# Optimization experiments

Hardware: AMD Instinct MI355X
Metric: run time of the kernel (lower is better)

The kernel has to match this reference:

```python
import jax, jax.numpy as jnp
import numpy as np

IN_CH = 128
OUT_CH = 256
KSIZE = 3
DOWN = 2
WSCALE_GAIN = 1.0
LR_MUL = 1.0
ACT_GAIN = float(np.sqrt(2.0))  # lrelu def_gain
CONV_CLAMP = 256.0
LRELU_SLOPE = 0.2


def _setup_filter():
    # upfirdn2d.setup_filter([1,3,3,1]): normalize 1D then outer product -> 2D
    f1 = jnp.asarray([1.0, 3.0, 3.0, 1.0], dtype=jnp.float32)
    f1 = f1 / jnp.sum(f1)
    f2 = jnp.outer(f1, f1)  # [4,4]
    return f2


def setup_inputs() -> dict:
    key = jax.random.key(0)
    k1, k2 = jax.random.split(key)
    x = jax.random.normal(k1, (16, IN_CH, 256, 256), dtype=jnp.float32)
    weight = jax.random.normal(k2, (OUT_CH, IN_CH, KSIZE, KSIZE), dtype=jnp.float32)
    bias = jnp.zeros((OUT_CH,), dtype=jnp.float32)
    return {"x": x, "weight": weight, "bias": bias}


def reference(x, weight, bias):
    # runtime_gain = 1.0
    fan_in = KSIZE * KSIZE * IN_CH
    wscale = WSCALE_GAIN / np.sqrt(fan_in) * LR_MUL  # use_wscale=True
    w = weight * jnp.float32(wscale)
    b = bias * jnp.float32(LR_MUL)

    # filter_padding for k=3, fh=fw=4, down=2 -> (2,2,2,2) as (left,right,top,bottom)
    pad = (KSIZE // 2 + (4 - DOWN + 1) // 2, KSIZE // 2 + (4 - DOWN) // 2)
    # upfirdn2d(x, f, down=1, padding): pad then correlate with flipped filter
    f2 = _setup_filter()
    f2 = f2[::-1, ::-1]  # flip (symmetric here, kept for faithfulness)
    C = x.shape[1]
    fk = jnp.broadcast_to(f2[None, None], (C, 1, 4, 4))  # depthwise kernel
    x = lax.pad_fn(x, pad) if False else jnp.pad(x, ((0, 0), (0, 0), (pad[1], pad[0]) if False else (pad[0], pad[1]), (pad[0], pad[1])))
    x = jax.lax.conv_general_dilated(
        x, fk, window_strides=(1, 1), padding='VALID',
        dimension_numbers=('NCHW', 'OIHW', 'NCHW'),
        feature_group_count=C)

    # strided conv2d, padding=0, stride=down
    x = jax.lax.conv_general_dilated(
        x, w, window_strides=(DOWN, DOWN), padding='VALID',
        dimension_numbers=('NCHW', 'OIHW', 'NCHW'))

    # fused bias + lrelu + gain + clamp
    x = x + b[None, :, None, None]
    x = jnp.where(x >= 0, x, x * jnp.float32(LRELU_SLOPE)) * jnp.float32(ACT_GAIN)
    x = jnp.clip(x, -jnp.float32(CONV_CLAMP), jnp.float32(CONV_CLAMP))
    return x
```

## Files before the change

### kernel.cpp

```cpp
#include <hip/hip_runtime.h>

typedef __attribute__((ext_vector_type(8))) short bf16x8;
typedef __attribute__((ext_vector_type(4))) float f32x4;
typedef __attribute__((ext_vector_type(2))) float f32x2;
typedef __attribute__((ext_vector_type(4))) unsigned int u32x4;

static __device__ __forceinline__ unsigned short f2bf(float f) {
    union { float f; unsigned u; } v; v.f = f;
    return (unsigned short)((v.u + 0x7FFFu + ((v.u >> 16) & 1u)) >> 16);
}

static __device__ __forceinline__ void g2l16(const void* g, void* l) {
    __builtin_amdgcn_global_load_lds(
        (const __attribute__((address_space(1))) unsigned int*)g,
        (__attribute__((address_space(3))) unsigned int*)l, 16, 0, 0);
}

__global__ void prep_weights(const float* __restrict__ w, unsigned short* __restrict__ wp) {
    int t = blockIdx.x * 256 + threadIdx.x;
    const float wscale = 0.02946278254943948f;
    int cw = t & 31;
    int oc = (t >> 5) & 255;
    int cr = t >> 13;
    int ch = cr / 9;
    int rs = cr - ch * 9;
    int r  = rs / 3;
    int s  = rs - r * 3;
    int c  = ch * 32 + cw;
    wp[t] = f2bf(w[((oc * 128 + c) * 3 + r) * 3 + s] * wscale);
}

#define BRW(ROW) {                                                             \
    int _xr = xr0 + (ROW);                                                     \
    int _xc = _xr < 0 ? 0 : (_xr > 255 ? 255 : _xr);                           \
    float _rm = (_xr == _xc) ? 0.125f : 0.0f;                                  \
    const float* _q0 = p0lo + (_xc << 8);                                      \
    const float* _h0p = p0hi + (_xc << 8);                                     \
    const float* _q1 = p1lo + (_xc << 8);                                      \
    const float* _h1p = p1hi + (_xc << 8);                                     \
    f32x4 _l0, _l1; f32x2 _h0, _h1;                                            \
    __builtin_memcpy(&_l0, _q0, 16); __builtin_memcpy(&_h0, _h0p, 8);          \
    __builtin_memcpy(&_l1, _q1, 16); __builtin_memcpy(&_h1, _h1p, 8);          \
    float w00 = eL ? 0.f : _l0.x,  w01 = eL ? 0.f : _l0.y;                     \
    float w02 = eL ? _l0.x : _l0.z, w03 = eL ? _l0.y : _l0.w;                  \
    float w04 = eR ? 0.f : (eL ? _l0.z : _h0.x);                               \
    float w05 = eR ? 0.f : (eL ? _l0.w : _h0.y);                               \
    float w10 = eL ? 0.f : _l1.x,  w11 = eL ? 0.f : _l1.y;                     \
    float w12 = eL ? _l1.x : _l1.z, w13 = eL ? _l1.y : _l1.w;                  \
    float w14 = eR ? 0.f : (eL ? _l1.z : _h1.x);                               \
    float w15 = eR ? 0.f : (eL ? _l1.w : _h1.y);                               \
    hA0[(ROW) & 3] = (w00 + 3.f * (w01 + w02) + w03) * _rm;                    \
    hB0[(ROW) & 3] = (w01 + 3.f * (w02 + w03) + w04) * _rm;                    \
    hC0[(ROW) & 3] = (w02 + 3.f * (w03 + w04) + w05) * _rm;                    \
    hA1[(ROW) & 3] = (w10 + 3.f * (w11 + w12) + w13) * _rm;                    \
    hB1[(ROW) & 3] = (w11 + 3.f * (w12 + w13) + w14) * _rm;                    \
    hC1[(ROW) & 3] = (w12 + 3.f * (w13 + w14) + w15) * _rm;                    \
}
#define BWV(ROW) {                                                             \
    float vA0 = (hA0[(ROW-3)&3] + 3.f*(hA0[(ROW-2)&3]+hA0[(ROW-1)&3]) + hA0[(ROW)&3]) * 0.125f; \
    float vA1 = (hA1[(ROW-3)&3] + 3.f*(hA1[(ROW-2)&3]+hA1[(ROW-1)&3]) + hA1[(ROW)&3]) * 0.125f; \
    float vB0 = (hB0[(ROW-3)&3] + 3.f*(hB0[(ROW-2)&3]+hB0[(ROW-1)&3]) + hB0[(ROW)&3]) * 0.125f; \
    float vB1 = (hB1[(ROW-3)&3] + 3.f*(hB1[(ROW-2)&3]+hB1[(ROW-1)&3]) + hB1[(ROW)&3]) * 0.125f; \
    unsigned _rb = (unsigned)(ROW - 3) * 2112u;                                \
    *(unsigned*)(blds + _rb + o0) = (unsigned)f2bf(vA0) | ((unsigned)f2bf(vA1) << 16); \
    *(unsigned*)(blds + _rb + o1) = (unsigned)f2bf(vB0) | ((unsigned)f2bf(vB1) << 16); \
    if (a15) {                                                                 \
        float vC0 = (hC0[(ROW-3)&3] + 3.f*(hC0[(ROW-2)&3]+hC0[(ROW-1)&3]) + hC0[(ROW)&3]) * 0.125f; \
        float vC1 = (hC1[(ROW-3)&3] + 3.f*(hC1[(ROW-2)&3]+hC1[(ROW-1)&3]) + hC1[(ROW)&3]) * 0.125f; \
        *(unsigned*)(blds + _rb + o2) = (unsigned)f2bf(vC0) | ((unsigned)f2bf(vC1) << 16); \
    }                                                                          \
}

__global__ __launch_bounds__(512, 4)
void blur_rec(const float* __restrict__ x, unsigned char* __restrict__ bm) {
    __shared__ __align__(16) unsigned char blds[17 * 2112];

    const int braw = blockIdx.x;
    const int bx   = ((braw & 7) << 10) | (braw >> 3);
    const int cg   = bx & 3;
    const int tile = (bx >> 2) & 127;
    const int n    = bx >> 9;
    const int u0   = (tile >> 3) * 8;
    const int v0   = (tile & 7) * 16;
    const int tid  = threadIdx.x;
    const int a    = tid & 15;
    const int chp  = (tid >> 4) & 15;
    const int h    = tid >> 8;
    const bool a15 = (a == 15);
    const int wc   = 2 * v0 - 2 + 2 * a;
    const bool eL  = (v0 == 0 && a == 0);
    const bool eR  = (v0 == 112 && a15);
    const int colLo = eL ? 0 : wc;
    const int colHi = eR ? 248 : (wc + 4);
    const float* plane0 = x + (size_t)(n * 128 + cg * 32 + 2 * chp) * 65536;
    const float* p0lo = plane0 + colLo;
    const float* p0hi = plane0 + colHi;
    const float* p1lo = p0lo + 65536;
    const float* p1hi = p0hi + 65536;
    const int xr0 = 2 * u0 - 2;

    const int J0 = 2 * a, J1 = 2 * a + 1;
    const unsigned cb2 = (unsigned)(chp & 3) * 4u;
    const unsigned o0 = (unsigned)((J0 ^ ((J0 >> 1) & 1)) * 64)
                      + ((((unsigned)chp >> 2) ^ (((unsigned)J0 >> 2) & 3u)) << 4) + cb2;
    const unsigned o1 = (unsigned)((J1 ^ ((J1 >> 1) & 1)) * 64)
                      + ((((unsigned)chp >> 2) ^ (((unsigned)J1 >> 2) & 3u)) << 4) + cb2;
    const unsigned o2 = 2048u + (((unsigned)chp >> 2) << 4) + cb2;

    {
        float hA0[4], hB0[4], hC0[4], hA1[4], hB1[4], hC1[4];
        if (h == 0) {
            BRW(0) BRW(1) BRW(2)
            BRW(3)  BWV(3)   BRW(4)  BWV(4)   BRW(5)  BWV(5)
            BRW(6)  BWV(6)   BRW(7)  BWV(7)   BRW(8)  BWV(8)
            BRW(9)  BWV(9)   BRW(10) BWV(10)  BRW(11) BWV(11)
        } else {
            BRW(9) BRW(10) BRW(11)
            BRW(12) BWV(12)  BRW(13) BWV(13)  BRW(14) BWV(14)
            BRW(15) BWV(15)  BRW(16) BWV(16)  BRW(17) BWV(17)
            BRW(18) BWV(18)  BRW(19) BWV(19)
        }
    }
    __syncthreads();
    unsigned char* dst = bm + (size_t)bx * 35904u;
    #pragma unroll
    for (int k = 0; k < 5; ++k) {
        int sl = tid + 512 * k;
        if (sl < 2244)
            *(u32x4*)(dst + (unsigned)sl * 16u) = *(const u32x4*)(blds + (unsigned)sl * 16u);
    }
}

#define MF __builtin_amdgcn_mfma_f32_16x16x32_bf16
#define WLOAD2(S0, S1, KOFF) {                                                 \
    const unsigned short* _wn = wbase + (size_t)(KOFF) * 8192;                 \
    S0 = *(const bf16x8*)(_wn); S1 = *(const bf16x8*)(_wn + 512);              \
}
#define CSTEP8(BUF, ADRS, R, S0, S1) {                                         \
    const unsigned char* _ab = lds + (BUF) + (ADRS) + (R) * 2112;              \
    bf16x8 a0 = *(const bf16x8*)(_ab);                                         \
    bf16x8 a1 = *(const bf16x8*)(_ab +  4224);                                 \
    bf16x8 a2 = *(const bf16x8*)(_ab +  8448);                                 \
    bf16x8 a3 = *(const bf16x8*)(_ab + 12672);                                 \
    bf16x8 a4 = *(const bf16x8*)(_ab + 16896);                                 \
    bf16x8 a5 = *(const bf16x8*)(_ab + 21120);                                 \
    bf16x8 a6 = *(const bf16x8*)(_ab + 25344);                                 \
    bf16x8 a7 = *(const bf16x8*)(_ab + 29568);                                 \
    __builtin_amdgcn_s_setprio(1);                                             \
    acc[0][0]=MF(a0,S0,acc[0][0],0,0,0); acc[0][1]=MF(a0,S1,acc[0][1],0,0,0);  \
    acc[1][0]=MF(a1,S0,acc[1][0],0,0,0); acc[1][1]=MF(a1,S1,acc[1][1],0,0,0);  \
    acc[2][0]=MF(a2,S0,acc[2][0],0,0,0); acc[2][1]=MF(a2,S1,acc[2][1],0,0,0);  \
    acc[3][0]=MF(a3,S0,acc[3][0],0,0,0); acc[3][1]=MF(a3,S1,acc[3][1],0,0,0);  \
    acc[4][0]=MF(a4,S0,acc[4][0],0,0,0); acc[4][1]=MF(a4,S1,acc[4][1],0,0,0);  \
    acc[5][0]=MF(a5,S0,acc[5][0],0,0,0); acc[5][1]=MF(a5,S1,acc[5][1],0,0,0);  \
    acc[6][0]=MF(a6,S0,acc[6][0],0,0,0); acc[6][1]=MF(a6,S1,acc[6][1],0,0,0);  \
    acc[7][0]=MF(a7,S0,acc[7][0],0,0,0); acc[7][1]=MF(a7,S1,acc[7][1],0,0,0);  \
    __builtin_amdgcn_s_setprio(0);                                             \
}
#define CHUNK8(BUF, BASE, A0,A1, B0,B1)                                        \
    CSTEP8(BUF, adr0, 0, A0,A1) WLOAD2(A0,A1, (BASE)+2)                        \
    CSTEP8(BUF, adr1, 0, B0,B1) WLOAD2(B0,B1, (BASE)+3)                        \
    CSTEP8(BUF, adr2, 0, A0,A1) WLOAD2(A0,A1, (BASE)+4)                        \
    CSTEP8(BUF, adr0, 1, B0,B1) WLOAD2(B0,B1, (BASE)+5)                        \
    CSTEP8(BUF, adr1, 1, A0,A1) WLOAD2(A0,A1, (BASE)+6)                        \
    CSTEP8(BUF, adr2, 1, B0,B1) WLOAD2(B0,B1, (BASE)+7)                        \
    CSTEP8(BUF, adr0, 2, A0,A1) WLOAD2(A0,A1, (BASE)+8)                        \
    CSTEP8(BUF, adr1, 2, B0,B1) WLOAD2(B0,B1, (BASE)+9)                        \
    CSTEP8(BUF, adr2, 2, A0,A1) WLOAD2(A0,A1, (BASE)+10)
#define CHUNK8_LAST(BUF, BASE, A0,A1, B0,B1)                                   \
    CSTEP8(BUF, adr0, 0, A0,A1) WLOAD2(A0,A1, (BASE)+2)                        \
    CSTEP8(BUF, adr1, 0, B0,B1) WLOAD2(B0,B1, (BASE)+3)                        \
    CSTEP8(BUF, adr2, 0, A0,A1) WLOAD2(A0,A1, (BASE)+4)                        \
    CSTEP8(BUF, adr0, 1, B0,B1) WLOAD2(B0,B1, (BASE)+5)                        \
    CSTEP8(BUF, adr1, 1, A0,A1) WLOAD2(A0,A1, (BASE)+6)                        \
    CSTEP8(BUF, adr2, 1, B0,B1) WLOAD2(B0,B1, (BASE)+7)                        \
    CSTEP8(BUF, adr0, 2, A0,A1) WLOAD2(A0,A1, (BASE)+8)                        \
    CSTEP8(BUF, adr1, 2, B0,B1)                                                \
    CSTEP8(BUF, adr2, 2, A0,A1)

__global__ __launch_bounds__(512, 4)
void conv_stage2(const unsigned char* __restrict__ bm, const unsigned short* __restrict__ wp,
                 const float* __restrict__ bias, float* __restrict__ out) {
    __shared__ __align__(16) unsigned char lds[2 * 35904];

    const int bx = blockIdx.x;
    const int n  = bx >> 7;
    const int tt = bx & 127;
    const int u0 = (tt >> 3) * 8;
    const int v0 = (tt & 7) * 16;

    const int tid  = threadIdx.x;
    const int lane = tid & 63;
    const int wid  = tid >> 6;
    const int g    = lane >> 4;
    const int wq   = lane & 15;

    const unsigned char* rec = bm + (size_t)((n * 128 + tt) * 4) * 35904u;

#define STAGE(BUF, CG) {                                                       \
    const unsigned char* _src = rec + (size_t)(CG) * 35904u;                   \
    _Pragma("unroll")                                                          \
    for (int k = 0; k < 4; ++k)                                                \
        g2l16(_src + (unsigned)(tid + 512 * k) * 16u,                          \
              lds + (BUF) + (unsigned)(tid + 512 * k) * 16u);                  \
    if (tid < 196)                                                             \
        g2l16(_src + (unsigned)(tid + 2048) * 16u,                             \
              lds + (BUF) + (unsigned)(tid + 2048) * 16u);                     \
}

    unsigned adr0, adr1, adr2;
    {
        #pragma unroll
        for (int s = 0; s < 3; ++s) {
            unsigned bj = 2u * (unsigned)wq + (unsigned)s;
            unsigned av = (bj ^ ((bj >> 1) & 1u)) * 64u
                        + (((unsigned)g ^ ((bj >> 2) & 3u)) << 4);
            if (s == 0) adr0 = av; else if (s == 1) adr1 = av; else adr2 = av;
        }
    }

    const unsigned short* wbase = wp + (size_t)(wid * 32 + wq) * 32 + g * 8;
    bf16x8 WA0, WA1, WB0, WB1;
    WLOAD2(WA0, WA1, 0)
    WLOAD2(WB0, WB1, 1)

    f32x4 acc[8][2];
    #pragma unroll
    for (int i = 0; i < 8; ++i) {
        acc[i][0] = (f32x4){0.f, 0.f, 0.f, 0.f};
        acc[i][1] = (f32x4){0.f, 0.f, 0.f, 0.f};
    }

    STAGE(0, 0)
    __syncthreads();

    STAGE(35904, 1)
    CHUNK8(0, 0, WA0, WA1, WB0, WB1)
    __syncthreads();

    STAGE(0, 2)
    CHUNK8(35904, 9, WB0, WB1, WA0, WA1)
    __syncthreads();

    STAGE(35904, 3)
    CHUNK8(0, 18, WA0, WA1, WB0, WB1)
    __syncthreads();

    CHUNK8_LAST(35904, 27, WB0, WB1, WA0, WA1)

    const float gain = 1.4142135623730951f;
    #pragma unroll
    for (int nf = 0; nf < 2; ++nf) {
        const int ocg = wid * 32 + nf * 16 + wq;
        const float bb = bias[ocg];
        #pragma unroll
        for (int mf = 0; mf < 8; ++mf) {
            f32x4 o;
            #pragma unroll
            for (int i = 0; i < 4; ++i) {
                float z = acc[mf][nf][i] + bb;
                z = (z >= 0.f ? z : 0.2f * z) * gain;
                o[i] = fminf(fmaxf(z, -256.f), 256.f);
            }
            *(f32x4*)(out + (((size_t)n * 256 + ocg) * 128 + (u0 + mf)) * 128 + v0 + 4 * g) = o;
        }
    }
}

#define FROW(row) {                                                            \
    int xr  = xr0 + (row);                                                     \
    int xrc = xr < 0 ? 0 : (xr > 255 ? 255 : xr);                              \
    float rm = (xr == xrc) ? 0.125f : 0.0f;                                    \
    const float* p = q + (xrc << 8);                                           \
    f32x4 lo; f32x2 hi;                                                        \
    __builtin_memcpy(&lo, p, 16);                                              \
    __builtin_memcpy(&hi, p + 4, 8);                                           \
    hA[(row) & 3] = (lo.x + 3.f * (lo.y + lo.z) + lo.w) * rm;                  \
    hB[(row) & 3] = (lo.y + 3.f * (lo.z + lo.w) + hi.x) * rm;                  \
    hC[(row) & 3] = (lo.z + 3.f * (lo.w + hi.x) + hi.y) * rm;                  \
}
#define SROW(row) {                                                            \
    int xr = xr0 + (row);                                                      \
    float wv0=0.f,wv1=0.f,wv2=0.f,wv3=0.f,wv4=0.f,wv5=0.f;                     \
    if ((unsigned)xr < 256u) {                                                 \
        const float* p = q + (xr << 8);                                        \
        if ((unsigned)(wc + 0) < 256u) wv0 = p[0];                             \
        if ((unsigned)(wc + 1) < 256u) wv1 = p[1];                             \
        if ((unsigned)(wc + 2) < 256u) wv2 = p[2];                             \
        if ((unsigned)(wc + 3) < 256u) wv3 = p[3];                             \
        if ((unsigned)(wc + 4) < 256u) wv4 = p[4];                             \
        if ((unsigned)(wc + 5) < 256u) wv5 = p[5];                             \
    }                                                                          \
    hA[(row) & 3] = (wv0 + 3.f * (wv1 + wv2) + wv3) * 0.125f;                  \
    hB[(row) & 3] = (wv1 + 3.f * (wv2 + wv3) + wv4) * 0.125f;                  \
    hC[(row) & 3] = (wv2 + 3.f * (wv3 + wv4) + wv5) * 0.125f;                  \
}
#define VROW(row) {                                                            \
    float bv0 = (hA[(row - 3) & 3] + 3.f * (hA[(row - 2) & 3] + hA[(row - 1) & 3]) + hA[(row) & 3]) * 0.125f; \
    float bv1 = (hB[(row - 3) & 3] + 3.f * (hB[(row - 2) & 3] + hB[(row - 1) & 3]) + hB[(row) & 3]) * 0.125f; \
    unsigned rb = (unsigned)(row - 3) * 2640u;                                 \
    *(unsigned short*)(flds + rb + o0) = f2bf(bv0);                            \
    *(unsigned short*)(flds + rb + o1) = f2bf(bv1);                            \
    if (a == 15) {                                                             \
        float bv2 = (hC[(row - 3) & 3] + 3.f * (hC[(row - 2) & 3] + hC[(row - 1) & 3]) + hC[(row) & 3]) * 0.125f; \
        *(unsigned short*)(flds + rb + o2) = f2bf(bv2);                        \
    }                                                                          \
}
__global__ __launch_bounds__(512, 4)
void conv_blur_mfma(const float* __restrict__ x, const unsigned short* __restrict__ wp,
                    const float* __restrict__ bias, float* __restrict__ out) {
    __shared__ __align__(16) unsigned char flds[17 * 33 * 80];
    const int bx = blockIdx.x;
    const int n  = bx >> 7;
    const int tt = bx & 127;
    const int u0 = (tt >> 3) * 8;
    const int v0 = (tt & 7) * 16;
    const int tid  = threadIdx.x;
    const int lane = tid & 63;
    const int wid  = tid >> 6;
    const int wm   = wid >> 2;
    const int wn   = wid & 3;
    const int g    = lane >> 4;
    const int wq   = lane & 15;
    const int a   = tid & 15;
    const int chl = tid >> 4;
    const int wc  = 2 * v0 - 2 + 2 * a;
    const bool edge = (v0 == 0 && a == 0) || (v0 == 112 && a == 15);
    const float* planeBase = x + (size_t)(n * 128 + chl) * 65536;
    const int xr0 = 2 * u0 - 2;
    const unsigned chpart = (unsigned)(((chl >> 1) & 3) * 4 + (chl & 1) * 2);
    const unsigned q4 = (unsigned)(chl >> 3);
    const int c0 = 2 * a;
    const unsigned o0 = (unsigned)(c0 + 0) * 80u + ((q4 ^ (((unsigned)(c0 + 0) >> 3) & 3u)) << 4) + chpart;
    const unsigned o1 = (unsigned)(c0 + 1) * 80u + ((q4 ^ (((unsigned)(c0 + 1) >> 3) & 3u)) << 4) + chpart;
    const unsigned o2 = (unsigned)(c0 + 2) * 80u + ((q4 ^ (((unsigned)(c0 + 2) >> 3) & 3u)) << 4) + chpart;
    const unsigned short* wpL = wp + (size_t)(wn * 64 + wq) * 32 + g * 8;
    f32x4 acc[4][4];
    #pragma unroll
    for (int i = 0; i < 4; ++i)
        #pragma unroll
        for (int j = 0; j < 4; ++j)
            acc[i][j] = (f32x4){0.f, 0.f, 0.f, 0.f};
    for (int ch = 0; ch < 4; ++ch) {
        const float* q = planeBase + (size_t)ch * 32 * 65536 + wc;
        float hA[4], hB[4], hC[4];
        if (!edge) { FROW(0) FROW(1) FROW(2) }
        else       { SROW(0) SROW(1) SROW(2) }
        __syncthreads();
        if (!edge) {
            #pragma unroll
            for (int row = 3; row < 20; ++row) { FROW(row) VROW(row) }
        } else {
            #pragma unroll
            for (int row = 3; row < 20; ++row) { SROW(row) VROW(row) }
        }
        __syncthreads();
        const unsigned short* wpc = wpL + (size_t)ch * 9 * 8192;
        #pragma unroll 1
        for (int r = 0; r < 3; ++r) {
            #pragma unroll 1
            for (int s = 0; s < 3; ++s) {
                bf16x8 b0 = *(const bf16x8*)(wpc + 0 * 512);
                bf16x8 b1 = *(const bf16x8*)(wpc + 1 * 512);
                bf16x8 b2 = *(const bf16x8*)(wpc + 2 * 512);
                bf16x8 b3 = *(const bf16x8*)(wpc + 3 * 512);
                wpc += 8192;
                int bj = 2 * wq + s;
                unsigned cb = (unsigned)bj * 80u + ((unsigned)(g ^ ((bj >> 3) & 3)) << 4);
                #pragma unroll
                for (int mf = 0; mf < 4; ++mf) {
                    int bi = 2 * (wm * 4 + mf) + r;
                    bf16x8 afrag = *(const bf16x8*)(flds + (unsigned)bi * 2640u + cb);
                    acc[mf][0] = MF(afrag, b0, acc[mf][0], 0, 0, 0);
                    acc[mf][1] = MF(afrag, b1, acc[mf][1], 0, 0, 0);
                    acc[mf][2] = MF(afrag, b2, acc[mf][2], 0, 0, 0);
                    acc[mf][3] = MF(afrag, b3, acc[mf][3], 0, 0, 0);
                }
            }
        }
    }
    const float gain = 1.4142135623730951f;
    #pragma unroll
    for (int nf = 0; nf < 4; ++nf) {
        int ocg = wn * 64 + nf * 16 + wq;
        float bv = bias[ocg];
        #pragma unroll
        for (int mf = 0; mf < 4; ++mf) {
            int u = u0 + wm * 4 + mf;
            f32x4 o;
            #pragma unroll
            for (int i = 0; i < 4; ++i) {
                float z = acc[mf][nf][i] + bv;
                z = (z >= 0.f ? z : 0.2f * z) * gain;
                o[i] = fminf(fmaxf(z, -256.f), 256.f);
            }
            *(f32x4*)(out + (((size_t)n * 256 + ocg) * 128 + u) * 128 + v0 + 4 * g) = o;
        }
    }
}

extern "C" void kernel_launch(void* const* d_in, const int* in_sizes, int n_in,
                              void* d_out, int out_size, void* d_ws, size_t ws_size,
                              hipStream_t stream) {
    const float* x    = (const float*)d_in[0];
    const float* w    = (const float*)d_in[1];
    const float* bias = (const float*)d_in[2];
    unsigned short* wp = (unsigned short*)d_ws;
    float* out = (float*)d_out;

    const size_t BM_BYTES = (size_t)8192 * 35904u;
    const size_t NEED = 589824u + BM_BYTES;
    prep_weights<<<1152, 256, 0, stream>>>(w, wp);
    if (ws_size >= NEED) {
        unsigned char* bm = (unsigned char*)d_ws + 589824;
        blur_rec<<<8192, 512, 0, stream>>>(x, bm);
        conv_stage2<<<2048, 512, 0, stream>>>(bm, wp, bias, out);
    } else {
        conv_blur_mfma<<<2048, 512, 0, stream>>>(x, wp, bias, out);
    }
}
```

Baseline: 421.3 us.

## Blur taller tiles per block with ring-buffered LDS to cut halo recompute

The blur_rec kernel now has each block process 16 output rows, where before it processed 8 rows split across two half-blocks that each recomputed 3 overlapping halo rows. A single 256-thread pass streams through 36 input rows. LDS shrinks to an 8-row ring buffer that is flushed to global memory every 4 rows, with a barrier before each flush. The intermediate record layout doubles in size per tile, and conv_stage2 addresses it with a 16-row offset for odd tiles. This removes the redundant halo reads and blur math and improves occupancy, at the cost of many more block syncs and less parallelism inside each block.

Result: no change. 422.0 us (+0.1%).

```diff
diff --git a/kernel.cpp b/kernel.cpp
--- a/kernel.cpp
+++ b/kernel.cpp
@@ -61,7 +61,7 @@
     float vA1 = (hA1[(ROW-3)&3] + 3.f*(hA1[(ROW-2)&3]+hA1[(ROW-1)&3]) + hA1[(ROW)&3]) * 0.125f; \
     float vB0 = (hB0[(ROW-3)&3] + 3.f*(hB0[(ROW-2)&3]+hB0[(ROW-1)&3]) + hB0[(ROW)&3]) * 0.125f; \
     float vB1 = (hB1[(ROW-3)&3] + 3.f*(hB1[(ROW-2)&3]+hB1[(ROW-1)&3]) + hB1[(ROW)&3]) * 0.125f; \
-    unsigned _rb = (unsigned)(ROW - 3) * 2112u;                                \
+    unsigned _rb = (unsigned)(((ROW) - 3) & 7) * 2112u;                        \
     *(unsigned*)(blds + _rb + o0) = (unsigned)f2bf(vA0) | ((unsigned)f2bf(vA1) << 16); \
     *(unsigned*)(blds + _rb + o1) = (unsigned)f2bf(vB0) | ((unsigned)f2bf(vB1) << 16); \
     if (a15) {                                                                 \
@@ -70,22 +70,34 @@
         *(unsigned*)(blds + _rb + o2) = (unsigned)f2bf(vC0) | ((unsigned)f2bf(vC1) << 16); \
     }                                                                          \
 }
-
-__global__ __launch_bounds__(512, 4)
+#define DUMP4(T0) {                                                            \
+    __syncthreads();                                                           \
+    _Pragma("unroll")                                                          \
+    for (int k = 0; k < 3; ++k) {                                              \
+        int sl = tid + 256 * k;                                                \
+        if (sl < 528) {                                                        \
+            int rr = sl / 132;                                                 \
+            int un = sl - rr * 132;                                            \
+            *(u32x4*)(dst + (unsigned)((T0) + rr) * 2112u + (unsigned)un * 16u) = \
+                *(const u32x4*)(blds + (unsigned)((((T0) + rr) & 7)) * 2112u + (unsigned)un * 16u); \
+        }                                                                      \
+    }                                                                          \
+}
+
+__global__ __launch_bounds__(256, 6)
 void blur_rec(const float* __restrict__ x, unsigned char* __restrict__ bm) {
-    __shared__ __align__(16) unsigned char blds[17 * 2112];
+    __shared__ __align__(16) unsigned char blds[8 * 2112];
 
     const int braw = blockIdx.x;
-    const int bx   = ((braw & 7) << 10) | (braw >> 3);
+    const int bx   = ((braw & 7) << 9) | (braw >> 3);
     const int cg   = bx & 3;
-    const int tile = (bx >> 2) & 127;
-    const int n    = bx >> 9;
-    const int u0   = (tile >> 3) * 8;
+    const int tile = (bx >> 2) & 63;
+    const int n    = bx >> 8;
+    const int u0   = (tile >> 3) * 16;
     const int v0   = (tile & 7) * 16;
     const int tid  = threadIdx.x;
     const int a    = tid & 15;
-    const int chp  = (tid >> 4) & 15;
-    const int h    = tid >> 8;
+    const int chp  = tid >> 4;
     const bool a15 = (a == 15);
     const int wc   = 2 * v0 - 2 + 2 * a;
     const bool eL  = (v0 == 0 && a == 0);
@@ -107,27 +119,23 @@
                       + ((((unsigned)chp >> 2) ^ (((unsigned)J1 >> 2) & 3u)) << 4) + cb2;
     const unsigned o2 = 2048u + (((unsigned)chp >> 2) << 4) + cb2;
 
-    {
-        float hA0[4], hB0[4], hC0[4], hA1[4], hB1[4], hC1[4];
-        if (h == 0) {
-            BRW(0) BRW(1) BRW(2)
-            BRW(3)  BWV(3)   BRW(4)  BWV(4)   BRW(5)  BWV(5)
-            BRW(6)  BWV(6)   BRW(7)  BWV(7)   BRW(8)  BWV(8)
-            BRW(9)  BWV(9)   BRW(10) BWV(10)  BRW(11) BWV(11)
-        } else {
-            BRW(9) BRW(10) BRW(11)
-            BRW(12) BWV(12)  BRW(13) BWV(13)  BRW(14) BWV(14)
-            BRW(15) BWV(15)  BRW(16) BWV(16)  BRW(17) BWV(17)
-            BRW(18) BWV(18)  BRW(19) BWV(19)
-        }
-    }
+    unsigned char* dst = bm + (size_t)bx * 69696u;
+    float hA0[4], hB0[4], hC0[4], hA1[4], hB1[4], hC1[4];
+
+    BRW(0) BRW(1) BRW(2)
+    BRW(3)  BWV(3)   BRW(4)  BWV(4)   BRW(5)  BWV(5)   BRW(6)  BWV(6)   DUMP4(0)
+    BRW(7)  BWV(7)   BRW(8)  BWV(8)   BRW(9)  BWV(9)   BRW(10) BWV(10)  DUMP4(4)
+    BRW(11) BWV(11)  BRW(12) BWV(12)  BRW(13) BWV(13)  BRW(14) BWV(14)  DUMP4(8)
+    BRW(15) BWV(15)  BRW(16) BWV(16)  BRW(17) BWV(17)  BRW(18) BWV(18)  DUMP4(12)
+    BRW(19) BWV(19)  BRW(20) BWV(20)  BRW(21) BWV(21)  BRW(22) BWV(22)  DUMP4(16)
+    BRW(23) BWV(23)  BRW(24) BWV(24)  BRW(25) BWV(25)  BRW(26) BWV(26)  DUMP4(20)
+    BRW(27) BWV(27)  BRW(28) BWV(28)  BRW(29) BWV(29)  BRW(30) BWV(30)  DUMP4(24)
+    BRW(31) BWV(31)  BRW(32) BWV(32)  BRW(33) BWV(33)  BRW(34) BWV(34)  DUMP4(28)
+    BRW(35) BWV(35)
     __syncthreads();
-    unsigned char* dst = bm + (size_t)bx * 35904u;
-    #pragma unroll
-    for (int k = 0; k < 5; ++k) {
-        int sl = tid + 512 * k;
-        if (sl < 2244)
-            *(u32x4*)(dst + (unsigned)sl * 16u) = *(const u32x4*)(blds + (unsigned)sl * 16u);
+    if (tid < 132) {
+        *(u32x4*)(dst + 32u * 2112u + (unsigned)tid * 16u) =
+            *(const u32x4*)(blds + (unsigned)tid * 16u);
     }
 }
 
@@ -195,10 +203,12 @@
     const int g    = lane >> 4;
     const int wq   = lane & 15;
 
-    const unsigned char* rec = bm + (size_t)((n * 128 + tt) * 4) * 35904u;
+    const unsigned char* rec = bm
+        + (size_t)((n * 64 + (tt >> 4) * 8 + (tt & 7)) * 4) * 69696u
+        + ((tt & 8) ? 16u * 2112u : 0u);
 
 #define STAGE(BUF, CG) {                                                       \
-    const unsigned char* _src = rec + (size_t)(CG) * 35904u;                   \
+    const unsigned char* _src = rec + (size_t)(CG) * 69696u;                   \
     _Pragma("unroll")                                                          \
     for (int k = 0; k < 4; ++k)                                                \
         g2l16(_src + (unsigned)(tid + 512 * k) * 16u,                          \
@@ -408,12 +418,12 @@
     unsigned short* wp = (unsigned short*)d_ws;
     float* out = (float*)d_out;
 
-    const size_t BM_BYTES = (size_t)8192 * 35904u;
+    const size_t BM_BYTES = (size_t)4096 * 69696u;
     const size_t NEED = 589824u + BM_BYTES;
     prep_weights<<<1152, 256, 0, stream>>>(w, wp);
     if (ws_size >= NEED) {
         unsigned char* bm = (unsigned char*)d_ws + 589824;
-        blur_rec<<<8192, 512, 0, stream>>>(x, bm);
+        blur_rec<<<4096, 256, 0, stream>>>(x, bm);
         conv_stage2<<<2048, 512, 0, stream>>>(bm, wp, bias, out);
     } else {
         conv_blur_mfma<<<2048, 512, 0, stream>>>(x, wp, bias, out);
```
